# Optimization experiments

Hardware: AMD Instinct MI355X
Metric: run time of the kernel (lower is better)

The kernel has to match this reference:

```python
import jax, jax.numpy as jnp
import numpy as np

B, H, W, D = 8, 64, 64, 1024


def setup_inputs() -> dict:
    key = jax.random.key(0)
    ks = jax.random.split(key, 10)
    s = 0.02
    return {
        "x": jax.random.normal(ks[0], (B, H, W, D), dtype=jnp.float32),
        "Wq": jax.random.normal(ks[1], (D, D), dtype=jnp.float32) * s,
        "bq": jnp.zeros((D,), dtype=jnp.float32),
        "Wk": jax.random.normal(ks[2], (D, D), dtype=jnp.float32) * s,
        "bk": jnp.zeros((D,), dtype=jnp.float32),
        "Wv": jax.random.normal(ks[3], (D, D), dtype=jnp.float32) * s,
        "bv": jnp.zeros((D,), dtype=jnp.float32),
        "Wo": jax.random.normal(ks[4], (D, D), dtype=jnp.float32) * s,
        "bo": jnp.zeros((D,), dtype=jnp.float32),
        "sigma": jnp.ones((1,), dtype=jnp.float32),
    }


def _dist(n, dtype):
    i = jnp.arange(n)
    return jnp.square(i[:, None] - i[None, :]).astype(dtype)


def reference(x, Wq, bq, Wk, bk, Wv, bv, Wo, bo, sigma):
    b, h, w, d = x.shape
    gw = 1.0 / (2.0 * jnp.square(sigma))  # scalar (shape [1])
    q = jnp.einsum('bhwd,ed->bhwe', x, Wq) + bq
    k = jnp.einsum('bhwd,ed->bhwe', x, Wk) + bk
    v = jnp.einsum('bhwd,ed->bhwe', x, Wv) + bv
    # row attention: attend across width within each row
    r_qk = jnp.einsum('bhwd,bhkd->bhwk', q, k) - gw[0] * _dist(w, x.dtype)
    r_attn = jax.nn.softmax(r_qk, axis=-1)               # [b,h,w,w]
    r_out = jnp.einsum('bhwk,bhkd->bhwd', r_attn, v)
    # column attention: attend across height within each column
    c_qk = jnp.einsum('bhwd,bgwd->bwhg', q, k) - gw[0] * _dist(h, x.dtype)
    c_attn = jax.nn.softmax(c_qk, axis=-1)               # [b,w,h,h]
    c_out = jnp.einsum('bwhg,bgwd->bhwd', c_attn, v)
    out = r_out + c_out
    return jnp.einsum('bhwd,ed->bhwe', out, Wo) + bo
```

## Files before the change

### kernel.cpp

```cpp
#include <hip/hip_runtime.h>


typedef _Float16 f16;
typedef __attribute__((ext_vector_type(8))) _Float16 f16x8;
typedef __attribute__((ext_vector_type(4))) float f32x4;

__global__ __launch_bounds__(256) void k_cvt_all(
    const float* __restrict__ x, const float* __restrict__ Wq,
    const float* __restrict__ Wk, const float* __restrict__ Wv,
    const float* __restrict__ Wo, f16* __restrict__ xb,
    f16* __restrict__ wqkv, f16* __restrict__ wob) {
  const int stride = gridDim.x * blockDim.x;
  const int X8 = 33554432 / 8;
  const int W8 = 1048576 / 8;
  const int total = X8 + 4 * W8;
  for (int i = blockIdx.x * blockDim.x + threadIdx.x; i < total; i += stride) {
    const float* src; f16* dst; int o8;
    if (i < X8) { src = x; dst = xb; o8 = i; }
    else {
      int j = i - X8; int seg = j >> 17; o8 = j & (W8 - 1);
      if (seg == 0)      { src = Wq; dst = wqkv; }
      else if (seg == 1) { src = Wk; dst = wqkv + 1048576; }
      else if (seg == 2) { src = Wv; dst = wqkv + 2097152; }
      else               { src = Wo; dst = wob; }
    }
    const float4* p = (const float4*)src + (size_t)o8 * 2;
    float4 a = p[0]; float4 b = p[1];
    f16x8 o;
    o[0]=(f16)a.x; o[1]=(f16)a.y; o[2]=(f16)a.z; o[3]=(f16)a.w;
    o[4]=(f16)b.x; o[5]=(f16)b.y; o[6]=(f16)b.z; o[7]=(f16)b.w;
    *(f16x8*)(dst + (size_t)o8 * 8) = o;
  }
}

template<bool C_F32>
__global__ __launch_bounds__(512, 2) void k_gemm256(const f16* __restrict__ A,
                                                    const f16* __restrict__ B,
                                                    const float* __restrict__ b0,
                                                    const float* __restrict__ b1,
                                                    const float* __restrict__ b2,
                                                    void* __restrict__ Cout,
                                                    int M, int N, int K) {
  __shared__ f16 smem[2][2][2][128 * 64];

  const int tid = threadIdx.x;
  const int lane = tid & 63;
  const int wid = tid >> 6;
  const int wr = wid >> 2;
  const int wc = wid & 3;
  const int lane_r = lane & 15;
  const int g = lane >> 4;

  const int nwg = gridDim.x;
  const int bid = blockIdx.x;
  const int swz = (bid & 7) * (nwg >> 3) + (bid >> 3);
  const int nbn = N >> 8;
  const int bm = swz / nbn, bn = swz % nbn;

  const int u0 = ((g) ^ (lane_r & 7)) * 8;
  const int u1 = ((4 + g) ^ (lane_r & 7)) * 8;
  const int arow = lane >> 3;
  const int acol = ((lane & 7) ^ (lane >> 3)) * 8;

  const f16* Ag[2] = { A + (size_t)(bm * 256) * K, A + (size_t)(bm * 256 + 128) * K };
  const f16* Bg[2] = { B + (size_t)(bn * 256) * K, B + (size_t)(bn * 256 + 128) * K };

  f32x4 acc[8][4];
#pragma unroll
  for (int i = 0; i < 8; ++i)
#pragma unroll
    for (int j = 0; j < 4; ++j) acc[i][j] = (f32x4){0.f, 0.f, 0.f, 0.f};

#define STAGE(gbase, kt, lbase)                                                     \
  {                                                                                 \
    _Pragma("unroll") for (int i_ = 0; i_ < 2; ++i_) {                              \
      const f16* g_ = (gbase) + (size_t)(wid * 16 + i_ * 8 + arow) * K + (kt) * 64 + acol; \
      __builtin_amdgcn_global_load_lds(                                             \
          (const __attribute__((address_space(1))) void*)g_,                        \
          (__attribute__((address_space(3))) void*)((lbase) + (wid * 16 + i_ * 8) * 64), \
          16, 0, 0);                                                                \
    }                                                                               \
  }

#define MFMAQ(q)                                                                    \
  _Pragma("unroll") for (int mm = 0; mm < 2; ++mm)                                  \
  _Pragma("unroll") for (int n = 0; n < 4; ++n) {                                   \
    acc[(q)*2 + mm][n] = __builtin_amdgcn_mfma_f32_16x16x32_f16(afrag[mm][0], bfrag[n][0], acc[(q)*2 + mm][n], 0, 0, 0); \
    acc[(q)*2 + mm][n] = __builtin_amdgcn_mfma_f32_16x16x32_f16(afrag[mm][1], bfrag[n][1], acc[(q)*2 + mm][n], 0, 0, 0); \
  }

#define READ_A(q)                                                                   \
  _Pragma("unroll") for (int mm = 0; mm < 2; ++mm) {                                \
    const int rb_ = ((q)*32 + mm * 16 + lane_r) * 64;                               \
    afrag[mm][0] = *(const f16x8*)&As_[rb_ + u0];                                   \
    afrag[mm][1] = *(const f16x8*)&As_[rb_ + u1];                                   \
  }

#define KTILE(t, slot, mode)                                                        \
  {                                                                                 \
    f16* As_ = smem[slot][0][wr];                                                   \
    f16* Bs_ = smem[slot][1][wc >> 1];                                              \
    f16x8 bfrag[4][2], afrag[2][2];                                                 \
    _Pragma("unroll") for (int n = 0; n < 4; ++n) {                                 \
      const int rb_ = ((wc & 1) * 64 + n * 16 + lane_r) * 64;                       \
      bfrag[n][0] = *(const f16x8*)&Bs_[rb_ + u0];                                  \
      bfrag[n][1] = *(const f16x8*)&Bs_[rb_ + u1];                                  \
    }                                                                               \
    READ_A(0)                                                                       \
    if ((mode) >= 1) STAGE(Ag[0], (t) + 1, smem[(slot) ^ 1][0][0]);                 \
    asm volatile("s_waitcnt lgkmcnt(8)" ::: "memory");                              \
    __builtin_amdgcn_s_barrier();                                                   \
    asm volatile("s_waitcnt lgkmcnt(0)" ::: "memory");                              \
    __builtin_amdgcn_s_setprio(1);                                                  \
    MFMAQ(0)                                                                        \
    __builtin_amdgcn_s_setprio(0);                                                  \
    __builtin_amdgcn_s_barrier();                                                   \
    READ_A(1)                                                                       \
    if ((mode) >= 1) STAGE(Ag[1], (t) + 1, smem[(slot) ^ 1][0][1]);                 \
    __builtin_amdgcn_s_barrier();                                                   \
    asm volatile("s_waitcnt lgkmcnt(0)" ::: "memory");                              \
    __builtin_amdgcn_s_setprio(1);                                                  \
    MFMAQ(1)                                                                        \
    __builtin_amdgcn_s_setprio(0);                                                  \
    __builtin_amdgcn_s_barrier();                                                   \
    READ_A(2)                                                                       \
    if ((mode) == 2) STAGE(Bg[0], (t) + 2, smem[slot][1][0]);                       \
    __builtin_amdgcn_s_barrier();                                                   \
    asm volatile("s_waitcnt lgkmcnt(0)" ::: "memory");                              \
    __builtin_amdgcn_s_setprio(1);                                                  \
    MFMAQ(2)                                                                        \
    __builtin_amdgcn_s_setprio(0);                                                  \
    __builtin_amdgcn_s_barrier();                                                   \
    READ_A(3)                                                                       \
    if ((mode) == 2) STAGE(Bg[1], (t) + 2, smem[slot][1][1]);                       \
    if ((mode) == 2) { asm volatile("s_waitcnt vmcnt(4)" ::: "memory"); }           \
    else if ((mode) == 1) { asm volatile("s_waitcnt vmcnt(0)" ::: "memory"); }      \
    __builtin_amdgcn_s_barrier();                                                   \
    asm volatile("s_waitcnt lgkmcnt(0)" ::: "memory");                              \
    __builtin_amdgcn_s_setprio(1);                                                  \
    MFMAQ(3)                                                                        \
    __builtin_amdgcn_s_setprio(0);                                                  \
    __builtin_amdgcn_s_barrier();                                                   \
  }

  const int nt = K >> 6;

  STAGE(Ag[0], 0, smem[0][0][0]);
  STAGE(Ag[1], 0, smem[0][0][1]);
  STAGE(Bg[0], 0, smem[0][1][0]);
  STAGE(Bg[1], 0, smem[0][1][1]);
  STAGE(Bg[0], 1, smem[1][1][0]);
  STAGE(Bg[1], 1, smem[1][1][1]);
  asm volatile("s_waitcnt vmcnt(4)" ::: "memory");
  __builtin_amdgcn_s_barrier();

  for (int t = 0; t + 3 < nt; t += 2) {
    KTILE(t, 0, 2)
    KTILE(t + 1, 1, 2)
  }
  KTILE(nt - 2, 0, 1)
  KTILE(nt - 1, 1, 0)

  const int mrow0 = bm * 256 + wr * 128 + (lane >> 4) * 4;
  const int ncol0 = bn * 256 + wc * 64 + (lane & 15);
#pragma unroll
  for (int n = 0; n < 4; ++n) {
    const int col = ncol0 + n * 16;
    const float* bp = (col < 1024) ? b0 : ((col < 2048) ? b1 : b2);
    const float bvv = bp[col & 1023];
#pragma unroll
    for (int mrep = 0; mrep < 8; ++mrep) {
#pragma unroll
      for (int r = 0; r < 4; ++r) {
        const int row = mrow0 + mrep * 16 + r;
        const float val = acc[mrep][n][r] + bvv;
        if (C_F32) ((float*)Cout)[(size_t)row * N + col] = val;
        else       ((f16*)Cout)[(size_t)row * N + col] = (f16)val;
      }
    }
  }
#undef KTILE
#undef READ_A
#undef MFMAQ
#undef STAGE
}

template<bool IS_COL>
__global__ __launch_bounds__(256) void k_attn(const f16* __restrict__ qkv,
                                              f16* __restrict__ attn,
                                              const float* __restrict__ sigma) {
  __shared__ union { float S[64][68]; f16 Vt[256][72]; } sm;
  __shared__ f16 P[64][72];

  const int tid = threadIdx.x;
  const int lane = tid & 63;
  const int wid = tid >> 6;
  const int blk = blockIdx.x;

  size_t tok0; int tstr;
  if (IS_COL) { tok0 = (size_t)(blk >> 6) * 4096 + (blk & 63); tstr = 64; }
  else        { tok0 = (size_t)blk * 64;                       tstr = 1;  }
  const size_t ibase = tok0 * 3072;  const int istr = tstr * 3072;
  const size_t obase = tok0 * 1024;  const int ostr = tstr * 1024;

  const float sg = sigma[0];
  const float gw = 0.5f / (sg * sg);

  const int m0 = wid * 16;
  const int lr = lane & 15;
  const int lq = lane >> 4;

  f32x4 sacc[4];
#pragma unroll
  for (int nt = 0; nt < 4; ++nt) sacc[nt] = (f32x4){0.f, 0.f, 0.f, 0.f};
  const f16* qp = qkv + ibase + (size_t)(m0 + lr) * istr + lq * 8;
  const f16* kp = qkv + ibase + 1024 + (size_t)lr * istr + lq * 8;
#pragma unroll 2
  for (int ks = 0; ks < 32; ++ks) {
    f16x8 af = *(const f16x8*)(qp + ks * 32);
#pragma unroll
    for (int nt = 0; nt < 4; ++nt) {
      f16x8 bfr = *(const f16x8*)(kp + (size_t)nt * 16 * istr + ks * 32);
      sacc[nt] = __builtin_amdgcn_mfma_f32_16x16x32_f16(af, bfr, sacc[nt], 0, 0, 0);
    }
  }
#pragma unroll
  for (int nt = 0; nt < 4; ++nt)
#pragma unroll
    for (int r = 0; r < 4; ++r) {
      const int row = m0 + lq * 4 + r;
      const int col = nt * 16 + lr;
      const float dd = (float)(row - col);
      sm.S[row][col] = sacc[nt][r] - gw * dd * dd;
    }
  __syncthreads();

  {
    const int r = tid >> 2, s4 = tid & 3;
    const float4* sp = (const float4*)&sm.S[r][s4 * 16];
    float vals[16];
#pragma unroll
    for (int j = 0; j < 4; ++j) {
      float4 t = sp[j];
      vals[j * 4 + 0] = t.x; vals[j * 4 + 1] = t.y; vals[j * 4 + 2] = t.z; vals[j * 4 + 3] = t.w;
    }
    float mx = vals[0];
#pragma unroll
    for (int j = 1; j < 16; ++j) mx = fmaxf(mx, vals[j]);
    mx = fmaxf(mx, __shfl_xor(mx, 1));
    mx = fmaxf(mx, __shfl_xor(mx, 2));
    float sum = 0.f;
#pragma unroll
    for (int j = 0; j < 16; ++j) { vals[j] = __expf(vals[j] - mx); sum += vals[j]; }
    sum += __shfl_xor(sum, 1);
    sum += __shfl_xor(sum, 2);
    const float inv = 1.f / sum;
#pragma unroll
    for (int j = 0; j < 16; ++j) P[r][s4 * 16 + j] = (f16)(vals[j] * inv);
  }
  __syncthreads();

  const f16x8 af0 = *(const f16x8*)&P[m0 + lr][lq * 8];
  const f16x8 af1 = *(const f16x8*)&P[m0 + lr][32 + lq * 8];

  const int kr = tid & 63;
  const int cg = tid >> 6;
  const f16* vp = qkv + ibase + 2048 + (size_t)kr * istr;

  for (int c = 0; c < 4; ++c) {
#pragma unroll
    for (int j8 = 0; j8 < 8; ++j8) {
      const int cl = cg * 64 + j8 * 8;
      f16x8 vv = *(const f16x8*)(vp + c * 256 + cl);
#pragma unroll
      for (int e = 0; e < 8; ++e) sm.Vt[cl + e][kr] = vv[e];
    }
    __syncthreads();
#pragma unroll
    for (int nt = 0; nt < 16; ++nt) {
      const f16x8 bf0 = *(const f16x8*)&sm.Vt[nt * 16 + lr][lq * 8];
      const f16x8 bf1 = *(const f16x8*)&sm.Vt[nt * 16 + lr][32 + lq * 8];
      f32x4 o = (f32x4){0.f, 0.f, 0.f, 0.f};
      o = __builtin_amdgcn_mfma_f32_16x16x32_f16(af0, bf0, o, 0, 0, 0);
      o = __builtin_amdgcn_mfma_f32_16x16x32_f16(af1, bf1, o, 0, 0, 0);
#pragma unroll
      for (int r = 0; r < 4; ++r) {
        const int row = m0 + lq * 4 + r;
        const int col = c * 256 + nt * 16 + lr;
        const size_t addr = obase + (size_t)row * ostr + col;
        float val = o[r];
        if (IS_COL) val += (float)attn[addr];
        attn[addr] = (f16)val;
      }
    }
    __syncthreads();
  }
}

extern "C" void kernel_launch(void* const* d_in, const int* in_sizes, int n_in,
                              void* d_out, int out_size, void* d_ws, size_t ws_size,
                              hipStream_t stream) {
  const float* x  = (const float*)d_in[0];
  const float* Wq = (const float*)d_in[1];
  const float* bq = (const float*)d_in[2];
  const float* Wk = (const float*)d_in[3];
  const float* bk = (const float*)d_in[4];
  const float* Wv = (const float*)d_in[5];
  const float* bv = (const float*)d_in[6];
  const float* Wo = (const float*)d_in[7];
  const float* bo = (const float*)d_in[8];
  const float* sg = (const float*)d_in[9];

  const int M = 8 * 64 * 64;
  const size_t NE = (size_t)M * 1024;

  f16* xb   = (f16*)d_ws;
  f16* wqkv = xb + NE;
  f16* wob  = wqkv + 3 * 1024 * 1024;
  f16* qkv  = wob + 1024 * 1024;

  k_cvt_all<<<2048, 256, 0, stream>>>(x, Wq, Wk, Wv, Wo, xb, wqkv, wob);

  k_gemm256<false><<<(M / 256) * (3072 / 256), 512, 0, stream>>>(
      xb, wqkv, bq, bk, bv, qkv, M, 3072, 1024);

  f16* attn = xb;
  k_attn<false><<<512, 256, 0, stream>>>(qkv, attn, sg);
  k_attn<true><<<512, 256, 0, stream>>>(qkv, attn, sg);

  k_gemm256<true><<<(M / 256) * (1024 / 256), 512, 0, stream>>>(
      attn, wob, bo, bo, bo, (float*)d_out, M, 1024, 1024);
}
```

Baseline: 517.8 us.

## Restructure GEMM k-tile pipeline to issue all prefetches upfront with fewer barriers

Reworks the per-k-tile schedule of the fp16 MFMA GEMM. Each tile now waits on global loads and syncs once at the start, then issues all A and B prefetch stages together. After that it runs the four MFMA quarters back to back without the intermediate barriers and lgkm waits between them. This cuts synchronization overhead and keeps MFMAs dense at high priority. In exchange, LDS reads for later quarters rely on implicit compiler waits, and the vmcnt accounting must still match the new load ordering, which risks correctness or races.

```diff
diff --git a/kernel.cpp b/kernel.cpp
--- a/kernel.cpp
+++ b/kernel.cpp
@@ -96,51 +96,38 @@
     afrag[mm][1] = *(const f16x8*)&As_[rb_ + u1];                                   \
   }
 
-#define KTILE(t, slot, mode)                                                        \
+#define KTILE(t, slot, vm, st)                                                      \
   {                                                                                 \
     f16* As_ = smem[slot][0][wr];                                                   \
     f16* Bs_ = smem[slot][1][wc >> 1];                                              \
     f16x8 bfrag[4][2], afrag[2][2];                                                 \
+    asm volatile("s_waitcnt vmcnt(%0)" :: "n"(vm) : "memory");                      \
+    __builtin_amdgcn_s_barrier();                                                   \
     _Pragma("unroll") for (int n = 0; n < 4; ++n) {                                 \
       const int rb_ = ((wc & 1) * 64 + n * 16 + lane_r) * 64;                       \
       bfrag[n][0] = *(const f16x8*)&Bs_[rb_ + u0];                                  \
       bfrag[n][1] = *(const f16x8*)&Bs_[rb_ + u1];                                  \
     }                                                                               \
     READ_A(0)                                                                       \
-    if ((mode) >= 1) STAGE(Ag[0], (t) + 1, smem[(slot) ^ 1][0][0]);                 \
-    asm volatile("s_waitcnt lgkmcnt(8)" ::: "memory");                              \
+    asm volatile("s_waitcnt lgkmcnt(4)" ::: "memory");                              \
     __builtin_amdgcn_s_barrier();                                                   \
-    asm volatile("s_waitcnt lgkmcnt(0)" ::: "memory");                              \
+    if ((st) >= 1) {                                                                \
+      STAGE(Ag[0], (t) + 1, smem[(slot) ^ 1][0][0]);                                \
+      STAGE(Ag[1], (t) + 1, smem[(slot) ^ 1][0][1]);                                \
+    }                                                                               \
+    if ((st) == 2) {                                                                \
+      STAGE(Bg[0], (t) + 2, smem[slot][1][0]);                                      \
+      STAGE(Bg[1], (t) + 2, smem[slot][1][1]);                                      \
+    }                                                                               \
     __builtin_amdgcn_s_setprio(1);                                                  \
     MFMAQ(0)                                                                        \
-    __builtin_amdgcn_s_setprio(0);                                                  \
-    __builtin_amdgcn_s_barrier();                                                   \
     READ_A(1)                                                                       \
-    if ((mode) >= 1) STAGE(Ag[1], (t) + 1, smem[(slot) ^ 1][0][1]);                 \
-    __builtin_amdgcn_s_barrier();                                                   \
-    asm volatile("s_waitcnt lgkmcnt(0)" ::: "memory");                              \
-    __builtin_amdgcn_s_setprio(1);                                                  \
     MFMAQ(1)                                                                        \
-    __builtin_amdgcn_s_setprio(0);                                                  \
-    __builtin_amdgcn_s_barrier();                                                   \
     READ_A(2)                                                                       \
-    if ((mode) == 2) STAGE(Bg[0], (t) + 2, smem[slot][1][0]);                       \
-    __builtin_amdgcn_s_barrier();                                                   \
-    asm volatile("s_waitcnt lgkmcnt(0)" ::: "memory");                              \
-    __builtin_amdgcn_s_setprio(1);                                                  \
     MFMAQ(2)                                                                        \
-    __builtin_amdgcn_s_setprio(0);                                                  \
-    __builtin_amdgcn_s_barrier();                                                   \
     READ_A(3)                                                                       \
-    if ((mode) == 2) STAGE(Bg[1], (t) + 2, smem[slot][1][1]);                       \
-    if ((mode) == 2) { asm volatile("s_waitcnt vmcnt(4)" ::: "memory"); }           \
-    else if ((mode) == 1) { asm volatile("s_waitcnt vmcnt(0)" ::: "memory"); }      \
-    __builtin_amdgcn_s_barrier();                                                   \
-    asm volatile("s_waitcnt lgkmcnt(0)" ::: "memory");                              \
-    __builtin_amdgcn_s_setprio(1);                                                  \
     MFMAQ(3)                                                                        \
     __builtin_amdgcn_s_setprio(0);                                                  \
-    __builtin_amdgcn_s_barrier();                                                   \
   }
 
   const int nt = K >> 6;
@@ -151,15 +138,13 @@
   STAGE(Bg[1], 0, smem[0][1][1]);
   STAGE(Bg[0], 1, smem[1][1][0]);
   STAGE(Bg[1], 1, smem[1][1][1]);
-  asm volatile("s_waitcnt vmcnt(4)" ::: "memory");
-  __builtin_amdgcn_s_barrier();
 
   for (int t = 0; t + 3 < nt; t += 2) {
-    KTILE(t, 0, 2)
-    KTILE(t + 1, 1, 2)
-  }
-  KTILE(nt - 2, 0, 1)
-  KTILE(nt - 1, 1, 0)
+    KTILE(t, 0, 4, 2)
+    KTILE(t + 1, 1, 4, 2)
+  }
+  KTILE(nt - 2, 0, 4, 1)
+  KTILE(nt - 1, 1, 0, 0)
 
   const int mrow0 = bm * 256 + wr * 128 + (lane >> 4) * 4;
   const int ncol0 = bn * 256 + wc * 64 + (lane & 15);
```

Result: no change. 512.6 us (-1.0%).
